# Performance work log

Measured on AMD Instinct MI355X. Metric: run time of the kernel, lower is better.

## Reference

```python
import jax, jax.numpy as jnp
import numpy as np

N = 100000
E = 1600000
L = 128   # latent_size
H = 128   # hidden_size
O = 128   # output_size


def setup_inputs() -> dict:
    key = jax.random.key(0)
    ks = jax.random.split(key, 16)
    s = 1.0 / np.sqrt(H)
    inp = {
        "z": jax.random.normal(ks[0], (N, L), dtype=jnp.float32),
        "edge_index": jax.random.randint(ks[1], (2, E), 0, N, dtype=jnp.int64),
        # LSTM params (torch order: i, f, g, o)
        "W_ih": jax.random.uniform(ks[2], (4 * H, L), jnp.float32, -s, s),
        "W_hh": jax.random.uniform(ks[3], (4 * H, H), jnp.float32, -s, s),
        "b_ih": jax.random.uniform(ks[4], (4 * H,), jnp.float32, -s, s),
        "b_hh": jax.random.uniform(ks[5], (4 * H,), jnp.float32, -s, s),
        # GCNConv weights (x @ W + b)
        "W1": jax.random.uniform(ks[6], (H, H), jnp.float32, -s, s),
        "b1": jnp.zeros((H,), jnp.float32),
        "W2": jax.random.uniform(ks[7], (H, H), jnp.float32, -s, s),
        "b2": jnp.zeros((H,), jnp.float32),
        # final Linear
        "W3": jax.random.uniform(ks[8], (O, H), jnp.float32, -s, s),
        "b3": jax.random.uniform(ks[9], (O,), jnp.float32, -s, s),
    }
    return inp


def _gcn_conv(x, W, b, src, dst, norm, n_nodes):
    # x: [N, H]; src/dst/norm: [E+N] (self-loops included)
    h = x @ W                                   # [N, H] transform first (H==H)
    msg = h[src] * norm[:, None]                # gather + edge scale
    out = jax.ops.segment_sum(msg, dst, num_segments=n_nodes)  # scatter-add
    return out + b


def _lstm_step(z, W_ih, W_hh, b_ih, b_hh):
    # single time-step, h0 = c0 = 0
    gates = z @ W_ih.T + (jnp.zeros((1, H), z.dtype) @ W_hh.T) + b_ih + b_hh
    i, f, g, o = jnp.split(gates, 4, axis=-1)
    c = jax.nn.sigmoid(i) * jnp.tanh(g)         # f * c0 == 0
    return jax.nn.sigmoid(o) * jnp.tanh(c)


def reference(z, edge_index, W_ih, W_hh, b_ih, b_hh, W1, b1, W2, b2, W3, b3):
    n = z.shape[0]
    # add self-loops (PyG GCNConv default)
    loop = jnp.arange(n, dtype=edge_index.dtype)
    src = jnp.concatenate([edge_index[0], loop])
    dst = jnp.concatenate([edge_index[1], loop])
    # symmetric normalization: deg from dst (incoming, incl. self-loop)
    deg = jax.ops.segment_sum(jnp.ones_like(dst, dtype=z.dtype), dst, num_segments=n)
    dinv = jnp.where(deg > 0, jax.lax.rsqrt(deg), 0.0)
    norm = dinv[src] * dinv[dst]

    h = _lstm_step(z, W_ih, W_hh, b_ih, b_hh)
    x = jax.nn.relu(_gcn_conv(h, W1, b1, src, dst, norm, n))
    x = _gcn_conv(x, W2, b2, src, dst, norm, n)
    return jax.nn.relu(x @ W3.T + b3)
```

## Files before the change

kernel.cpp:

```cpp
#include <hip/hip_runtime.h>
#include <math.h>

typedef __attribute__((ext_vector_type(8))) short short8;
typedef __attribute__((ext_vector_type(4))) float floatx4;

#define HDIM 128
#define NPB 256
#define BKMAX 1024
#define CHUNK 8192
#define STAGE_CAP 8192

__device__ __forceinline__ float bf2f(unsigned short u) {
    unsigned int x = ((unsigned int)u) << 16;
    float f;
    __builtin_memcpy(&f, &x, 4);
    return f;
}
__device__ __forceinline__ unsigned short f2bf(float f) {
    unsigned int x;
    __builtin_memcpy(&x, &f, 4);
    unsigned int r = (x + 0x7fffu + ((x >> 16) & 1u)) >> 16;
    return (unsigned short)r;
}
__device__ __forceinline__ void split1(float v, unsigned short& hi, unsigned short& lo) {
    unsigned int x;
    __builtin_memcpy(&x, &v, 4);
    hi = (unsigned short)(x >> 16);
    lo = f2bf(v - bf2f(hi));
}
__device__ __forceinline__ float fast_sigmoid(float x) {
    return 1.0f / (1.0f + __expf(-x));
}
__device__ __forceinline__ float fast_tanh(float x) {
    float ax = fabsf(x);
    float e = __expf(2.0f * ax);
    float t = 1.0f - 2.0f / (e + 1.0f);
    return copysignf(t, x);
}

__device__ __forceinline__ void gload_lds16(const void* g, void* lds) {
    __builtin_amdgcn_global_load_lds(
        (const __attribute__((address_space(1))) unsigned int*)g,
        (__attribute__((address_space(3))) unsigned int*)lds, 16, 0, 0);
}

__global__ void prep_weights_kernel(const float* __restrict__ Wih,
                                    const float* __restrict__ W1,
                                    const float* __restrict__ W2,
                                    const float* __restrict__ W3,
                                    const float* __restrict__ bih,
                                    const float* __restrict__ bhh,
                                    unsigned short* __restrict__ Wihh, unsigned short* __restrict__ Wihl,
                                    unsigned short* __restrict__ W1h,  unsigned short* __restrict__ W1l,
                                    unsigned short* __restrict__ W2h,  unsigned short* __restrict__ W2l,
                                    unsigned short* __restrict__ W3h,  unsigned short* __restrict__ W3l,
                                    float* __restrict__ bsum) {
    int i = blockIdx.x * 256 + threadIdx.x;
    unsigned short h, l;
    if (i < 65536) {
        split1(Wih[i], h, l);
        Wihh[i] = h; Wihl[i] = l;
    } else if (i < 81920) {
        int t = i - 65536, r = t >> 7, c = t & 127;
        split1(W1[r * HDIM + c], h, l);
        W1h[c * HDIM + r] = h; W1l[c * HDIM + r] = l;
    } else if (i < 98304) {
        int t = i - 81920, r = t >> 7, c = t & 127;
        split1(W2[r * HDIM + c], h, l);
        W2h[c * HDIM + r] = h; W2l[c * HDIM + r] = l;
    } else if (i < 114688) {
        int t = i - 98304;
        split1(W3[t], h, l);
        W3h[t] = h; W3l[t] = l;
    } else if (i < 115200) {
        int t = i - 114688;
        bsum[t] = bih[t] + bhh[t];
    }
}

__global__ __launch_bounds__(256)
void bucket_hist_kernel(const int* __restrict__ ei, int* __restrict__ bcnt,
                        long E, int K) {
    __shared__ int h[BKMAX];
    const int tid = threadIdx.x;
    for (int i = tid; i < K; i += 256) h[i] = 0;
    __syncthreads();
    const long base = (long)blockIdx.x * CHUNK;
#pragma unroll
    for (int j = 0; j < CHUNK / 256; ++j) {
        long e = base + j * 256 + tid;
        if (e < E) atomicAdd(&h[((unsigned)ei[E + e]) >> 8], 1);
    }
    __syncthreads();
    for (int i = tid; i < K; i += 256) {
        int c = h[i];
        if (c) atomicAdd(&bcnt[i], c);
    }
}

__global__ __launch_bounds__(1024)
void scan_buckets_kernel(const int* __restrict__ bcnt, int* __restrict__ gbase,
                         int* __restrict__ gcur, int* __restrict__ offs,
                         int K, int N, int Etot) {
    __shared__ int buf[1024];
    const int t = threadIdx.x;
    const int v = (t < K) ? bcnt[t] : 0;
    buf[t] = v;
    __syncthreads();
    for (int off = 1; off < 1024; off <<= 1) {
        int x = buf[t];
        int y = (t >= off) ? buf[t - off] : 0;
        __syncthreads();
        buf[t] = x + y;
        __syncthreads();
    }
    if (t < K) { gbase[t] = buf[t] - v; gcur[t] = buf[t] - v; }
    if (t == 0) { gbase[K] = Etot; offs[N] = Etot; }
}

__global__ __launch_bounds__(256)
void pair_scatter_kernel(const int* __restrict__ ei, int* __restrict__ gcur,
                         unsigned int* __restrict__ pairs, long E, int K) {
    __shared__ int h[BKMAX];
    __shared__ int cur[BKMAX];
    const int tid = threadIdx.x;
    for (int i = tid; i < K; i += 256) h[i] = 0;
    __syncthreads();
    const long base = (long)blockIdx.x * CHUNK;
#pragma unroll
    for (int j = 0; j < CHUNK / 256; ++j) {
        long e = base + j * 256 + tid;
        if (e < E) atomicAdd(&h[((unsigned)ei[E + e]) >> 8], 1);
    }
    __syncthreads();
    for (int i = tid; i < K; i += 256) {
        int c = h[i];
        cur[i] = c ? atomicAdd(&gcur[i], c) : 0;
    }
    __syncthreads();
#pragma unroll
    for (int j = 0; j < CHUNK / 256; ++j) {
        long e = base + j * 256 + tid;
        if (e < E) {
            unsigned int s = (unsigned int)ei[e];
            unsigned int d = (unsigned int)ei[E + e];
            int b = d >> 8;
            int pos = atomicAdd(&cur[b], 1);
            pairs[pos] = s | ((d & (NPB - 1)) << 24);
        }
    }
}

__global__ __launch_bounds__(256)
void bucket_csr_kernel(const unsigned int* __restrict__ pairs, const int* __restrict__ gbase,
                       int* __restrict__ offs, float* __restrict__ dinv,
                       int* __restrict__ srclist, int N) {
    __shared__ int cnt[NPB];
    __shared__ int red[NPB];
    __shared__ int cur[NPB];
    __shared__ int stage[STAGE_CAP];
    const int tid = threadIdx.x;
    const int b = blockIdx.x;
    const int node0 = b << 8;
    const int nn = min(NPB, N - node0);
    const int ebeg = gbase[b];
    const int eend = gbase[b + 1];
    const int ne = eend - ebeg;

    cnt[tid] = 0;
    __syncthreads();
    for (int i = tid; i < ne; i += 256)
        atomicAdd(&cnt[pairs[ebeg + i] >> 24], 1);
    __syncthreads();
    const int myc = cnt[tid];
    red[tid] = myc;
    __syncthreads();
    for (int off = 1; off < NPB; off <<= 1) {
        int x = red[tid];
        int y = (tid >= off) ? red[tid - off] : 0;
        __syncthreads();
        red[tid] = x + y;
        __syncthreads();
    }
    const int loff = red[tid] - myc;
    if (tid < nn) {
        offs[node0 + tid] = ebeg + loff;
        dinv[node0 + tid] = rsqrtf((float)myc + 1.0f);
    }
    cur[tid] = loff;
    __syncthreads();

    if (ne <= STAGE_CAP) {
        for (int i = tid; i < ne; i += 256) {
            unsigned int p = pairs[ebeg + i];
            int pos = atomicAdd(&cur[p >> 24], 1);
            stage[pos] = (int)(p & 0xFFFFFFu);
        }
        __syncthreads();
        for (int i = tid; i < ne; i += 256)
            srclist[ebeg + i] = stage[i];
    } else {
        for (int i = tid; i < ne; i += 256) {
            unsigned int p = pairs[ebeg + i];
            int pos = atomicAdd(&cur[p >> 24], 1);
            srclist[ebeg + pos] = (int)(p & 0xFFFFFFu);
        }
    }
}

__device__ __forceinline__ void stage_swz(const unsigned short* __restrict__ g,
                                          long rowBase, long maxRow, int kOff,
                                          unsigned short* lds, int nrows, int tid) {
    const int nchunks = nrows << 3;
    for (int L = tid; L < nchunks; L += 256) {
        int r = L >> 3, cS = L & 7;
        int cG = cS ^ (r & 7);
        long gr = rowBase + r;
        if (gr >= maxRow) gr = maxRow - 1;
        gload_lds16(g + gr * HDIM + kOff + cG * 8, lds + (long)L * 8);
    }
}
__device__ __forceinline__ int swz_off(int r, int c0) {
    return (r * 8 + (c0 ^ (r & 7))) * 8;
}

__global__ __launch_bounds__(256, 4)
void gemm_split(const unsigned short* __restrict__ Ah, const unsigned short* __restrict__ Al,
                const unsigned short* __restrict__ Bh, const unsigned short* __restrict__ Bl,
                float* __restrict__ outf, unsigned short* __restrict__ outb, long M,
                const float* __restrict__ rowScale,
                const float* __restrict__ bias, int mode)
{
    __shared__ unsigned short sBh[128 * 64], sBl[128 * 64];
    const int tid = threadIdx.x;
    const long rowBase = (long)blockIdx.x * 64;

    const int wave = tid >> 6;
    const int lane = tid & 63;
    const int quad = lane >> 4;
    const int l16  = lane & 15;
    const int arow = wave * 16 + l16;
    long ag = rowBase + arow;
    if (ag >= M) ag = M - 1;

    short8 rah[2][2], ral[2][2];
#pragma unroll
    for (int h = 0; h < 2; ++h)
#pragma unroll
        for (int kk = 0; kk < 2; ++kk) {
            const long o = ag * HDIM + h * 64 + kk * 32 + quad * 8;
            rah[h][kk] = *(const short8*)(Ah + o);
            ral[h][kk] = *(const short8*)(Al + o);
        }

    floatx4 acc[8];
#pragma unroll
    for (int i = 0; i < 8; ++i) acc[i] = (floatx4)0.0f;

    for (int h = 0; h < 2; ++h) {
        __syncthreads();
        stage_swz(Bh, 0, 128, h * 64, sBh, 128, tid);
        stage_swz(Bl, 0, 128, h * 64, sBl, 128, tid);
        __syncthreads();
#pragma unroll
        for (int kk = 0; kk < 2; ++kk) {
            const int c0 = kk * 4 + quad;
            short8 ah = rah[h][kk];
            short8 al = ral[h][kk];
#pragma unroll
            for (int ct = 0; ct < 8; ++ct) {
                const int bo = swz_off(ct * 16 + l16, c0);
                short8 bh = *(const short8*)(sBh + bo);
                short8 bl = *(const short8*)(sBl + bo);
                acc[ct] = __builtin_amdgcn_mfma_f32_16x16x32_bf16(ah, bh, acc[ct], 0, 0, 0);
                acc[ct] = __builtin_amdgcn_mfma_f32_16x16x32_bf16(ah, bl, acc[ct], 0, 0, 0);
                acc[ct] = __builtin_amdgcn_mfma_f32_16x16x32_bf16(al, bh, acc[ct], 0, 0, 0);
            }
        }
    }

#pragma unroll
    for (int ct = 0; ct < 8; ++ct) {
#pragma unroll
        for (int r = 0; r < 4; ++r) {
            long m = rowBase + wave * 16 + quad * 4 + r;
            if (m < M) {
                int n = ct * 16 + l16;
                float v = acc[ct][r];
                if (mode == 0) {
                    v *= rowScale[m];
                    outb[m * HDIM + n] = f2bf(v);
                } else {
                    v += bias[n];
                    v = fmaxf(v, 0.0f);
                    outf[m * HDIM + n] = v;
                }
            }
        }
    }
}

__global__ __launch_bounds__(256, 2)
void lstm_gemm_split(const float* __restrict__ Z,
                     const unsigned short* __restrict__ Wh, const unsigned short* __restrict__ Wl,
                     const float* __restrict__ bsum,
                     unsigned short* __restrict__ Hh, unsigned short* __restrict__ Hl, long M)
{
    __shared__ unsigned short sBh[2][128 * 64], sBl[2][128 * 64];
    const int tid = threadIdx.x;
    const long rowBase = (long)blockIdx.x * 64;

    const int wave = tid >> 6;
    const int lane = tid & 63;
    const int quad = lane >> 4;
    const int l16  = lane & 15;
    const int arow = wave * 16 + l16;
    long ag = rowBase + arow;
    if (ag >= M) ag = M - 1;

    short8 rah[2][2], ral[2][2];
#pragma unroll
    for (int h = 0; h < 2; ++h)
#pragma unroll
        for (int kk = 0; kk < 2; ++kk) {
            const float* p = Z + ag * HDIM + h * 64 + kk * 32 + quad * 8;
            float4 f0 = *(const float4*)p;
            float4 f1 = *(const float4*)(p + 4);
            float f[8] = {f0.x, f0.y, f0.z, f0.w, f1.x, f1.y, f1.z, f1.w};
#pragma unroll
            for (int e = 0; e < 8; ++e) {
                unsigned short hi, lo;
                split1(f[e], hi, lo);
                rah[h][kk][e] = (short)hi;
                ral[h][kk][e] = (short)lo;
            }
        }

    auto stage_phase = [&](int ph, int b) {
        const int g = ph >> 1, h = ph & 1;
        const int gateRow = (g == 0) ? 0 : ((g == 1) ? 256 : 384);
        const unsigned short* gh = Wh + (long)gateRow * HDIM + h * 64;
        const unsigned short* gl = Wl + (long)gateRow * HDIM + h * 64;
#pragma unroll
        for (int it = 0; it < 4; ++it) {
            int L = it * 256 + tid;
            int r = L >> 3, cS = L & 7, cG = cS ^ (r & 7);
            gload_lds16(gh + (long)r * HDIM + cG * 8, &sBh[b][L * 8]);
        }
#pragma unroll
        for (int it = 0; it < 4; ++it) {
            int L = it * 256 + tid;
            int r = L >> 3, cS = L & 7, cG = cS ^ (r & 7);
            gload_lds16(gl + (long)r * HDIM + cG * 8, &sBl[b][L * 8]);
        }
    };

    floatx4 acc[8];
    floatx4 st[8];
#pragma unroll
    for (int i = 0; i < 8; ++i) acc[i] = (floatx4)0.0f;

    stage_phase(0, 0);

#pragma unroll
    for (int ph = 0; ph < 6; ++ph) {
        const int b = ph & 1;
        if (ph < 5) stage_phase(ph + 1, b ^ 1);
        if (ph == 2) {
#pragma unroll
            for (int ct = 0; ct < 8; ++ct) {
                const float bb = bsum[ct * 16 + l16];
#pragma unroll
                for (int r = 0; r < 4; ++r)
                    st[ct][r] = fast_sigmoid(acc[ct][r] + bb);
                acc[ct] = (floatx4)0.0f;
            }
        } else if (ph == 4) {
#pragma unroll
            for (int ct = 0; ct < 8; ++ct) {
                const float bb = bsum[256 + ct * 16 + l16];
#pragma unroll
                for (int r = 0; r < 4; ++r) {
                    float cv = st[ct][r] * fast_tanh(acc[ct][r] + bb);
                    st[ct][r] = fast_tanh(cv);
                }
                acc[ct] = (floatx4)0.0f;
            }
        }
        if (ph < 5) asm volatile("s_waitcnt vmcnt(8)" ::: "memory");
        else        asm volatile("s_waitcnt vmcnt(0)" ::: "memory");
        __builtin_amdgcn_s_barrier();
        asm volatile("" ::: "memory");
#pragma unroll
        for (int kk = 0; kk < 2; ++kk) {
            const int c0 = kk * 4 + quad;
            short8 ah = rah[ph & 1 ? (ph >> 1, 1) : 1, 0][0];
            (void)ah;
            const int hh_ = ph & 1;
            short8 a_h = rah[hh_][kk];
            short8 a_l = ral[hh_][kk];
#pragma unroll
            for (int ct = 0; ct < 8; ++ct) {
                const int bo = swz_off(ct * 16 + l16, c0);
                short8 bh = *(const short8*)(&sBh[b][0] + bo);
                short8 bl = *(const short8*)(&sBl[b][0] + bo);
                acc[ct] = __builtin_amdgcn_mfma_f32_16x16x32_bf16(a_h, bh, acc[ct], 0, 0, 0);
                acc[ct] = __builtin_amdgcn_mfma_f32_16x16x32_bf16(a_h, bl, acc[ct], 0, 0, 0);
                acc[ct] = __builtin_amdgcn_mfma_f32_16x16x32_bf16(a_l, bh, acc[ct], 0, 0, 0);
            }
        }
        asm volatile("s_waitcnt lgkmcnt(0)" ::: "memory");
        __builtin_amdgcn_s_barrier();
        asm volatile("" ::: "memory");
    }

#pragma unroll
    for (int ct = 0; ct < 8; ++ct) {
        const float bb = bsum[384 + ct * 16 + l16];
#pragma unroll
        for (int r = 0; r < 4; ++r) {
            long m = rowBase + wave * 16 + quad * 4 + r;
            if (m < M) {
                float hv = fast_sigmoid(acc[ct][r] + bb) * st[ct][r];
                unsigned short hh, hl;
                split1(hv, hh, hl);
                int n = ct * 16 + l16;
                Hh[m * HDIM + n] = hh;
                Hl[m * HDIM + n] = hl;
            }
        }
    }
}

__global__ __launch_bounds__(256, 4)
void aggregate_kernel(const unsigned short* __restrict__ t, const int* __restrict__ srclist,
                      const int* __restrict__ offs, const float* __restrict__ dinv,
                      const float* __restrict__ bias, int doRelu,
                      unsigned short* __restrict__ Xh, unsigned short* __restrict__ Xl, long N)
{
    long node = (long)blockIdx.x * 4 + (threadIdx.x >> 6);
    if (node >= N) return;
    const int lane = threadIdx.x & 63;
    const int c = lane * 2;
    const int beg = offs[node];
    const int end = offs[node + 1];
    float s0[8], s1[8];
#pragma unroll
    for (int q = 0; q < 8; ++q) { s0[q] = 0.0f; s1[q] = 0.0f; }
    int j = beg;
    for (; j + 8 <= end; j += 8) {
        int srcs[8];
#pragma unroll
        for (int q = 0; q < 8; ++q) srcs[q] = srclist[j + q];
        unsigned int p[8];
#pragma unroll
        for (int q = 0; q < 8; ++q) p[q] = *(const unsigned int*)(t + (long)srcs[q] * HDIM + c);
#pragma unroll
        for (int q = 0; q < 8; ++q) {
            s0[q] += bf2f((unsigned short)(p[q] & 0xffffu));
            s1[q] += bf2f((unsigned short)(p[q] >> 16));
        }
    }
    for (; j + 4 <= end; j += 4) {
        int srcs[4];
#pragma unroll
        for (int q = 0; q < 4; ++q) srcs[q] = srclist[j + q];
#pragma unroll
        for (int q = 0; q < 4; ++q) {
            unsigned int p = *(const unsigned int*)(t + (long)srcs[q] * HDIM + c);
            s0[q] += bf2f((unsigned short)(p & 0xffffu));
            s1[q] += bf2f((unsigned short)(p >> 16));
        }
    }
    for (; j < end; ++j) {
        unsigned int p = *(const unsigned int*)(t + (long)srclist[j] * HDIM + c);
        s0[0] += bf2f((unsigned short)(p & 0xffffu));
        s1[0] += bf2f((unsigned short)(p >> 16));
    }
    const unsigned int ps = *(const unsigned int*)(t + node * HDIM + c);
    s0[0] += bf2f((unsigned short)(ps & 0xffffu));
    s1[0] += bf2f((unsigned short)(ps >> 16));
    float a0 = ((s0[0] + s0[1]) + (s0[2] + s0[3])) + ((s0[4] + s0[5]) + (s0[6] + s0[7]));
    float a1 = ((s1[0] + s1[1]) + (s1[2] + s1[3])) + ((s1[4] + s1[5]) + (s1[6] + s1[7]));
    const float d = dinv[node];
    float v0 = d * a0 + bias[c];
    float v1 = d * a1 + bias[c + 1];
    if (doRelu) { v0 = fmaxf(v0, 0.0f); v1 = fmaxf(v1, 0.0f); }
    unsigned short h0, l0, h1, l1;
    split1(v0, h0, l0);
    split1(v1, h1, l1);
    *(unsigned int*)(Xh + node * HDIM + c) = (unsigned int)h0 | ((unsigned int)h1 << 16);
    *(unsigned int*)(Xl + node * HDIM + c) = (unsigned int)l0 | ((unsigned int)l1 << 16);
}

extern "C" void kernel_launch(void* const* d_in, const int* in_sizes, int n_in,
                              void* d_out, int out_size, void* d_ws, size_t ws_size,
                              hipStream_t stream)
{
    const float* z   = (const float*)d_in[0];
    const int*   ei  = (const int*)d_in[1];
    const float* Wih = (const float*)d_in[2];
    const float* bih = (const float*)d_in[4];
    const float* bhh = (const float*)d_in[5];
    const float* W1  = (const float*)d_in[6];
    const float* b1  = (const float*)d_in[7];
    const float* W2  = (const float*)d_in[8];
    const float* b2  = (const float*)d_in[9];
    const float* W3  = (const float*)d_in[10];
    const float* b3  = (const float*)d_in[11];
    float* out = (float*)d_out;

    const long N = in_sizes[0] / HDIM;
    const long E = in_sizes[1] / 2;
    const int  K = (int)((N + NPB - 1) / NPB);

    char* ws = (char*)d_ws;
    size_t off = 0;
    auto alloc = [&](size_t bytes) {
        char* p = ws + off;
        off += (bytes + 255) & ~(size_t)255;
        return (void*)p;
    };
    int*   bcnt    = (int*)alloc(K * 4);
    int*   gbase   = (int*)alloc((K + 1) * 4);
    int*   gcur    = (int*)alloc(K * 4);
    int*   offs    = (int*)alloc((N + 1) * 4);
    float* dinv    = (float*)alloc(N * 4);
    unsigned int* pairs = (unsigned int*)alloc(E * 4);
    int*   srclist = (int*)alloc(E * 4);
    unsigned short* P1h = (unsigned short*)alloc(N * HDIM * 2);
    unsigned short* P1l = (unsigned short*)alloc(N * HDIM * 2);
    unsigned short* P2h = (unsigned short*)alloc(N * HDIM * 2);
    unsigned short* P2l = (unsigned short*)alloc(N * HDIM * 2);
    unsigned short* Tb  = (unsigned short*)alloc(N * HDIM * 2);
    unsigned short* Wihh = (unsigned short*)alloc(512 * HDIM * 2);
    unsigned short* Wihl = (unsigned short*)alloc(512 * HDIM * 2);
    unsigned short* W1h  = (unsigned short*)alloc(HDIM * HDIM * 2);
    unsigned short* W1l  = (unsigned short*)alloc(HDIM * HDIM * 2);
    unsigned short* W2h  = (unsigned short*)alloc(HDIM * HDIM * 2);
    unsigned short* W2l  = (unsigned short*)alloc(HDIM * HDIM * 2);
    unsigned short* W3h  = (unsigned short*)alloc(HDIM * HDIM * 2);
    unsigned short* W3l  = (unsigned short*)alloc(HDIM * HDIM * 2);
    float* bsum = (float*)alloc(512 * 4);

    const int gblocks = (int)((N + 63) / 64);
    const int ablocks = (int)((N + 3) / 4);
    const int cblocks = (int)((E + CHUNK - 1) / CHUNK);

    hipMemsetAsync(bcnt, 0, K * 4, stream);
    bucket_hist_kernel<<<cblocks, 256, 0, stream>>>(ei, bcnt, E, K);
    scan_buckets_kernel<<<1, 1024, 0, stream>>>(bcnt, gbase, gcur, offs, K, (int)N, (int)E);
    pair_scatter_kernel<<<cblocks, 256, 0, stream>>>(ei, gcur, pairs, E, K);
    bucket_csr_kernel<<<K, 256, 0, stream>>>(pairs, gbase, offs, dinv, srclist, (int)N);

    prep_weights_kernel<<<451, 256, 0, stream>>>(Wih, W1, W2, W3, bih, bhh,
                                                 Wihh, Wihl, W1h, W1l, W2h, W2l, W3h, W3l, bsum);

    lstm_gemm_split<<<gblocks, 256, 0, stream>>>(z, Wihh, Wihl, bsum, P2h, P2l, N);

    gemm_split<<<gblocks, 256, 0, stream>>>(P2h, P2l, W1h, W1l, nullptr, Tb, N, dinv, nullptr, 0);
    aggregate_kernel<<<ablocks, 256, 0, stream>>>(Tb, srclist, offs, dinv, b1, 1, P1h, P1l, N);

    gemm_split<<<gblocks, 256, 0, stream>>>(P1h, P1l, W2h, W2l, nullptr, Tb, N, dinv, nullptr, 0);
    aggregate_kernel<<<ablocks, 256, 0, stream>>>(Tb, srclist, offs, dinv, b2, 0, P2h, P2l, N);

    gemm_split<<<gblocks, 256, 0, stream>>>(P2h, P2l, W3h, W3l, out, nullptr, N, nullptr, b3, 1);
}
```

Before: 459.1 us.

## Fold second GCN weight and final linear into one precomputed matrix

Precomputes W23 = W2·W3ᵀ and a combined bias b2·W3ᵀ + b3 in a small prep kernel. The second GCN transform then uses W23, and its aggregation applies the combined bias and ReLU and writes fp32 output directly. This removes the final GEMM pass and its intermediate bf16 hi/lo buffers. Because the weights are reassociated, rounding changes slightly.

After: 440.1 us. 4.1% less time.

```diff
diff --git a/kernel.cpp b/kernel.cpp
--- a/kernel.cpp
+++ b/kernel.cpp
@@ -46,14 +46,10 @@
 
 __global__ void prep_weights_kernel(const float* __restrict__ Wih,
                                     const float* __restrict__ W1,
-                                    const float* __restrict__ W2,
-                                    const float* __restrict__ W3,
                                     const float* __restrict__ bih,
                                     const float* __restrict__ bhh,
                                     unsigned short* __restrict__ Wihh, unsigned short* __restrict__ Wihl,
                                     unsigned short* __restrict__ W1h,  unsigned short* __restrict__ W1l,
-                                    unsigned short* __restrict__ W2h,  unsigned short* __restrict__ W2l,
-                                    unsigned short* __restrict__ W3h,  unsigned short* __restrict__ W3l,
                                     float* __restrict__ bsum) {
     int i = blockIdx.x * 256 + threadIdx.x;
     unsigned short h, l;
@@ -64,17 +60,37 @@
         int t = i - 65536, r = t >> 7, c = t & 127;
         split1(W1[r * HDIM + c], h, l);
         W1h[c * HDIM + r] = h; W1l[c * HDIM + r] = l;
-    } else if (i < 98304) {
-        int t = i - 81920, r = t >> 7, c = t & 127;
-        split1(W2[r * HDIM + c], h, l);
-        W2h[c * HDIM + r] = h; W2l[c * HDIM + r] = l;
-    } else if (i < 114688) {
-        int t = i - 98304;
-        split1(W3[t], h, l);
-        W3h[t] = h; W3l[t] = l;
-    } else if (i < 115200) {
-        int t = i - 114688;
+    } else if (i < 82432) {
+        int t = i - 81920;
         bsum[t] = bih[t] + bhh[t];
+    }
+}
+
+__global__ void prep_w23_kernel(const float* __restrict__ W2,
+                                const float* __restrict__ W3,
+                                const float* __restrict__ b2,
+                                const float* __restrict__ b3,
+                                unsigned short* __restrict__ W23h,
+                                unsigned short* __restrict__ W23l,
+                                float* __restrict__ b23) {
+    int i = blockIdx.x * 256 + threadIdx.x;
+    if (i < 16384) {
+        int n = i >> 7, k = i & 127;
+        float s = 0.0f;
+#pragma unroll 8
+        for (int p = 0; p < 128; ++p)
+            s += W2[k * HDIM + p] * W3[n * HDIM + p];
+        unsigned short h, l;
+        split1(s, h, l);
+        W23h[n * HDIM + k] = h;
+        W23l[n * HDIM + k] = l;
+    } else if (i < 16512) {
+        int n = i - 16384;
+        float s = b3[n];
+#pragma unroll 8
+        for (int p = 0; p < 128; ++p)
+            s += b2[p] * W3[n * HDIM + p];
+        b23[n] = s;
     }
 }
 
@@ -391,12 +407,10 @@
         else        asm volatile("s_waitcnt vmcnt(0)" ::: "memory");
         __builtin_amdgcn_s_barrier();
         asm volatile("" ::: "memory");
+        const int hh_ = ph & 1;
 #pragma unroll
         for (int kk = 0; kk < 2; ++kk) {
             const int c0 = kk * 4 + quad;
-            short8 ah = rah[ph & 1 ? (ph >> 1, 1) : 1, 0][0];
-            (void)ah;
-            const int hh_ = ph & 1;
             short8 a_h = rah[hh_][kk];
             short8 a_l = ral[hh_][kk];
 #pragma unroll
@@ -436,7 +450,8 @@
 void aggregate_kernel(const unsigned short* __restrict__ t, const int* __restrict__ srclist,
                       const int* __restrict__ offs, const float* __restrict__ dinv,
                       const float* __restrict__ bias, int doRelu,
-                      unsigned short* __restrict__ Xh, unsigned short* __restrict__ Xl, long N)
+                      unsigned short* __restrict__ Xh, unsigned short* __restrict__ Xl,
+                      float* __restrict__ outF, long N)
 {
     long node = (long)blockIdx.x * 4 + (threadIdx.x >> 6);
     if (node >= N) return;
@@ -485,6 +500,13 @@
     const float d = dinv[node];
     float v0 = d * a0 + bias[c];
     float v1 = d * a1 + bias[c + 1];
+    if (outF) {
+        v0 = fmaxf(v0, 0.0f);
+        v1 = fmaxf(v1, 0.0f);
+        float2 o2 = {v0, v1};
+        *(float2*)(outF + node * HDIM + c) = o2;
+        return;
+    }
     if (doRelu) { v0 = fmaxf(v0, 0.0f); v1 = fmaxf(v1, 0.0f); }
     unsigned short h0, l0, h1, l1;
     split1(v0, h0, l0);
@@ -537,15 +559,14 @@
     unsigned short* Wihl = (unsigned short*)alloc(512 * HDIM * 2);
     unsigned short* W1h  = (unsigned short*)alloc(HDIM * HDIM * 2);
     unsigned short* W1l  = (unsigned short*)alloc(HDIM * HDIM * 2);
-    unsigned short* W2h  = (unsigned short*)alloc(HDIM * HDIM * 2);
-    unsigned short* W2l  = (unsigned short*)alloc(HDIM * HDIM * 2);
-    unsigned short* W3h  = (unsigned short*)alloc(HDIM * HDIM * 2);
-    unsigned short* W3l  = (unsigned short*)alloc(HDIM * HDIM * 2);
+    unsigned short* W23h = (unsigned short*)alloc(HDIM * HDIM * 2);
+    unsigned short* W23l = (unsigned short*)alloc(HDIM * HDIM * 2);
     float* bsum = (float*)alloc(512 * 4);
-
-    const int gblocks = (int)((N + 63) / 64);
-    const int ablocks = (int)((N + 3) / 4);
-    const int cblocks = (int)((E + CHUNK - 1) / CHUNK);
+    float* b23  = (float*)alloc(HDIM * 4);
+
+    const int gblocks  = (int)((N + 63) / 64);
+    const int ablocks  = (int)((N + 3) / 4);
+    const int cblocks  = (int)((E + CHUNK - 1) / CHUNK);
 
     hipMemsetAsync(bcnt, 0, K * 4, stream);
     bucket_hist_kernel<<<cblocks, 256, 0, stream>>>(ei, bcnt, E, K);
@@ -553,16 +574,17 @@
     pair_scatter_kernel<<<cblocks, 256, 0, stream>>>(ei, gcur, pairs, E, K);
     bucket_csr_kernel<<<K, 256, 0, stream>>>(pairs, gbase, offs, dinv, srclist, (int)N);
 
-    prep_weights_kernel<<<451, 256, 0, stream>>>(Wih, W1, W2, W3, bih, bhh,
-                                                 Wihh, Wihl, W1h, W1l, W2h, W2l, W3h, W3l, bsum);
+    prep_weights_kernel<<<322, 256, 0, stream>>>(Wih, W1, bih, bhh,
+                                                 Wihh, Wihl, W1h, W1l, bsum);
+    prep_w23_kernel<<<65, 256, 0, stream>>>(W2, W3, b2, b3, W23h, W23l, b23);
 
     lstm_gemm_split<<<gblocks, 256, 0, stream>>>(z, Wihh, Wihl, bsum, P2h, P2l, N);
 
     gemm_split<<<gblocks, 256, 0, stream>>>(P2h, P2l, W1h, W1l, nullptr, Tb, N, dinv, nullptr, 0);
-    aggregate_kernel<<<ablocks, 256, 0, stream>>>(Tb, srclist, offs, dinv, b1, 1, P1h, P1l, N);
-
-    gemm_split<<<gblocks, 256, 0, stream>>>(P1h, P1l, W2h, W2l, nullptr, Tb, N, dinv, nullptr, 0);
-    aggregate_kernel<<<ablocks, 256, 0, stream>>>(Tb, srclist, offs, dinv, b2, 0, P2h, P2l, N);
-
-    gemm_split<<<gblocks, 256, 0, stream>>>(P2h, P2l, W3h, W3l, out, nullptr, N, nullptr, b3, 1);
-}
+    aggregate_kernel<<<ablocks, 256, 0, stream>>>(Tb, srclist, offs, dinv, b1, 1,
+                                                  P1h, P1l, nullptr, N);
+
+    gemm_split<<<gblocks, 256, 0, stream>>>(P1h, P1l, W23h, W23l, nullptr, Tb, N, dinv, nullptr, 0);
+    aggregate_kernel<<<ablocks, 256, 0, stream>>>(Tb, srclist, offs, dinv, b23, 1,
+                                                  nullptr, nullptr, out, N);
+}
```
